# Kernel optimization log

Measured on AMD Instinct MI355X. Metric: run time of the kernel, lower is better.

## Reference

```python
import jax, jax.numpy as jnp
import numpy as np

B, S, D, H = 4, 2048, 1024, 16
HD = D // H  # head_dim = 64


def setup_inputs() -> dict:
    key = jax.random.key(0)
    ks = jax.random.split(key, 4)
    scale = 0.02
    return {
        "x": jax.random.normal(ks[0], (B, S, D), dtype=jnp.float32),
        "W_attn": jax.random.normal(ks[1], (D, 3 * D), dtype=jnp.float32) * scale,
        "b_attn": jnp.zeros((3 * D,), dtype=jnp.float32),
        "W_proj": jax.random.normal(ks[2], (D, D), dtype=jnp.float32) * scale,
        "b_proj": jnp.zeros((D,), dtype=jnp.float32),
    }


def reference(x, W_attn, b_attn, W_proj, b_proj):
    b, s, d = x.shape
    qkv = x @ W_attn + b_attn                      # [b, s, 3d]
    q, k, v = jnp.split(qkv, 3, axis=2)
    # [b, s, d] -> [b, h, s, hd]
    def to_heads(t):
        return t.reshape(b, s, H, HD).transpose(0, 2, 1, 3)
    q, k, v = to_heads(q), to_heads(k), to_heads(v)
    scores = jnp.einsum("bhqd,bhkd->bhqk", q, k) / jnp.sqrt(jnp.float32(HD))
    causal = jnp.tril(jnp.ones((s, s), dtype=bool))  # [s, s]
    scores = jnp.where(causal[None, None], scores, jnp.float32(-jnp.inf))
    probs = jax.nn.softmax(scores, axis=-1)
    y = jnp.einsum("bhqk,bhkd->bhqd", probs, v)    # [b, h, s, hd]
    y = y.transpose(0, 2, 1, 3).reshape(b, s, d)
    return y @ W_proj + b_proj
```

## Files before the change

### kernel.cpp

```cpp
#include <hip/hip_runtime.h>
#include <hip/hip_bf16.h>
#include <type_traits>

#define SQ    2048
#define DIM   1024
#define NH    16
#define HDIM  64
#define BATCH 4

typedef unsigned short u16;
typedef __bf16 bf16x8 __attribute__((ext_vector_type(8)));
typedef float  f32x4  __attribute__((ext_vector_type(4)));
typedef u16    u16x8  __attribute__((ext_vector_type(8)));

#define QSCALE 0.180336880f

__device__ __forceinline__ u16 f2bf(float f) {
  union { float f; unsigned u; } v; v.f = f;
  unsigned r = v.u + 0x7fffu + ((v.u >> 16) & 1u);
  return (u16)(r >> 16);
}

__device__ __forceinline__ float fast_exp2(float x) {
#if __has_builtin(__builtin_amdgcn_exp2f)
  return __builtin_amdgcn_exp2f(x);
#else
  float y;
  asm("v_exp_f32 %0, %1" : "=v"(y) : "v"(x));
  return y;
#endif
}

__device__ __forceinline__ void gll16(const u16* g, u16* l) {
  __builtin_amdgcn_global_load_lds((const __attribute__((address_space(1))) void*)g,
                                   (__attribute__((address_space(3))) void*)l,
                                   16, 0, 0);
}

__global__ __launch_bounds__(256)
void f32_to_bf16_vec(const float* __restrict__ in, u16* __restrict__ out, int n4)
{
  const int i = blockIdx.x * blockDim.x + threadIdx.x;
  if (i < n4) {
    const float4 v = ((const float4*)in)[i];
    ushort4 o;
    o.x = f2bf(v.x); o.y = f2bf(v.y); o.z = f2bf(v.z); o.w = f2bf(v.w);
    ((ushort4*)out)[i] = o;
  }
}

__global__ void transpose_f32_bf16(const float* __restrict__ in, u16* __restrict__ out,
                                   int R, int C)
{
  __shared__ u16 tile[32][33];
  const int bx = blockIdx.x * 32, by = blockIdx.y * 32;
  const int tx = threadIdx.x, ty = threadIdx.y;
  #pragma unroll
  for (int i = 0; i < 32; i += 8)
    tile[ty + i][tx] = f2bf(in[(size_t)(by + ty + i) * C + bx + tx]);
  __syncthreads();
  #pragma unroll
  for (int i = 0; i < 32; i += 8)
    out[(size_t)(bx + ty + i) * R + by + tx] = tile[tx][ty + i];
}

template<int MODE>
__global__ __launch_bounds__(256)
void gemm_bt(const u16* __restrict__ A, const u16* __restrict__ Bt,
             const float* __restrict__ bias, int K,
             u16* __restrict__ o0, u16* __restrict__ o1, float* __restrict__ of)
{
  __shared__ __align__(16) u16 A0[128 * 32], A1[128 * 32];
  __shared__ __align__(16) u16 B0[128 * 32], B1[128 * 32];

  const int t    = threadIdx.x;
  const int lane = t & 63, wave = t >> 6;
  const int l15  = lane & 15, quad = lane >> 4;
  const int wm   = (wave & 1) * 64, wn = (wave >> 1) * 64;
  const int m0   = blockIdx.y * 128, n0 = blockIdx.x * 128;

  const int srow = wave * 32 + (lane >> 2);
  const int scol = (lane & 3) * 8;

  f32x4 acc[4][4] = {};

  for (int k0 = 0; k0 < K; k0 += 64) {
    const u16* ga = A  + (size_t)(m0 + srow) * K + k0 + scol;
    const u16* gb = Bt + (size_t)(n0 + srow) * K + k0 + scol;
    gll16(ga,              &A0[(wave * 32)      * 32]);
    gll16(ga + 32,         &A1[(wave * 32)      * 32]);
    gll16(ga + 16 * K,     &A0[(wave * 32 + 16) * 32]);
    gll16(ga + 16 * K + 32,&A1[(wave * 32 + 16) * 32]);
    gll16(gb,              &B0[(wave * 32)      * 32]);
    gll16(gb + 32,         &B1[(wave * 32)      * 32]);
    gll16(gb + 16 * K,     &B0[(wave * 32 + 16) * 32]);
    gll16(gb + 16 * K + 32,&B1[(wave * 32 + 16) * 32]);
    __syncthreads();

    #pragma unroll
    for (int ks = 0; ks < 2; ++ks) {
      const u16* Als = ks ? A1 : A0;
      const u16* Bls = ks ? B1 : B0;
      bf16x8 af[4], bfr[4];
      #pragma unroll
      for (int i = 0; i < 4; ++i) af[i]  = *(const bf16x8*)&Als[(wm + 16*i + l15) * 32 + quad * 8];
      #pragma unroll
      for (int j = 0; j < 4; ++j) bfr[j] = *(const bf16x8*)&Bls[(wn + 16*j + l15) * 32 + quad * 8];
      #pragma unroll
      for (int i = 0; i < 4; ++i)
        #pragma unroll
        for (int j = 0; j < 4; ++j)
          acc[i][j] = (MODE == 2)
            ? __builtin_amdgcn_mfma_f32_16x16x32_bf16(bfr[j], af[i], acc[i][j], 0, 0, 0)
            : __builtin_amdgcn_mfma_f32_16x16x32_bf16(af[i], bfr[j], acc[i][j], 0, 0, 0);
    }
    __syncthreads();
  }

  if (MODE == 2) {
    #pragma unroll
    for (int j = 0; j < 4; ++j) {
      #pragma unroll
      for (int r = 0; r < 4; ++r) {
        const int d = n0 + wn + 16*j + quad * 4 + r;
        const float bn = bias[d];
        const int h = d >> 6, hd = d & 63;
        #pragma unroll
        for (int i = 0; i < 4; ++i) {
          const int m = m0 + wm + 16*i + l15;
          const int b = m >> 11, s = m & 2047;
          o0[(((size_t)(b * NH + h)) * HDIM + hd) * SQ + s] = f2bf(acc[i][j][r] + bn);
        }
      }
    }
  } else {
    #pragma unroll
    for (int j = 0; j < 4; ++j) {
      const int n = n0 + wn + 16*j + l15;
      const float bn = bias[n];
      #pragma unroll
      for (int i = 0; i < 4; ++i) {
        #pragma unroll
        for (int r = 0; r < 4; ++r) {
          const int m = m0 + wm + 16*i + quad * 4 + r;
          const float val = acc[i][j][r] + bn;
          if (MODE == 1) {
            const int sec = n >> 10, d = n & 1023;
            const int h = d >> 6, hd = d & 63;
            const int b = m >> 11, s = m & 2047;
            const int bh = b * NH + h;
            if (sec == 0) o0[((size_t)bh * SQ + s) * HDIM + hd] = f2bf(val * QSCALE);
            else          o1[((size_t)bh * SQ + s) * HDIM + hd] = f2bf(val);
          } else {
            of[(size_t)m * DIM + n] = val;
          }
        }
      }
    }
  }
}

__global__ __launch_bounds__(256)
void attn_fused(const u16* __restrict__ q_ws, const u16* __restrict__ k_ws,
                const u16* __restrict__ v_t, u16* __restrict__ y_ws)
{
  __shared__ __align__(16) u16 Kls[2][64 * 64];
  __shared__ __align__(16) u16 Vls[2][64 * 64];
  __shared__ __align__(16) u16 Pls[4][32 * 64];

  const int bh = blockIdx.x;
  const int p  = blockIdx.y;
  const int b = bh >> 4, h = bh & 15;
  const int t = threadIdx.x;
  const int lane = t & 63, wave = t >> 6;
  const int l15 = lane & 15, quad = lane >> 4;
  const int rx  = l15 & 7;
  const int cK0 = ((quad      ^ rx) << 3);
  const int cK1 = (((quad | 4) ^ rx) << 3);
  const int pswz = rx << 3;

  const u16* Q  = q_ws + (size_t)bh * SQ * HDIM;
  const u16* Kp = k_ws + (size_t)bh * SQ * HDIM;
  const u16* Vp = v_t  + (size_t)bh * HDIM * SQ;

  const int qtH = 15 - p, qtL = p;
  const int qrowH = qtH * 128 + wave * 32;
  const int qrowL = qtL * 128 + wave * 32;

  bf16x8 qf[4][2];
  #pragma unroll
  for (int qi = 0; qi < 2; ++qi)
    #pragma unroll
    for (int ks = 0; ks < 2; ++ks) {
      qf[qi][ks]     = *(const bf16x8*)&Q[(size_t)(qrowH + 16*qi + l15) * HDIM + ks * 32 + quad * 8];
      qf[2 + qi][ks] = *(const bf16x8*)&Q[(size_t)(qrowL + 16*qi + l15) * HDIM + ks * 32 + quad * 8];
    }

  f32x4 o[4][4] = {};
  float l_q[4] = {};

  const int r3   = lane >> 3;
  const int c8   = lane & 7;
  const int scol = ((c8 ^ r3) << 3);

  auto stage = [&](int kv0, int buf) {
    gll16(&Kp[(size_t)(kv0 + wave*16     + r3) * HDIM + scol], &Kls[buf][(wave*16    ) * 64]);
    gll16(&Kp[(size_t)(kv0 + wave*16 + 8 + r3) * HDIM + scol], &Kls[buf][(wave*16 + 8) * 64]);
    gll16(&Vp[(size_t)(wave*16     + r3) * SQ + kv0 + scol],   &Vls[buf][(wave*16    ) * 64]);
    gll16(&Vp[(size_t)(wave*16 + 8 + r3) * SQ + kv0 + scol],   &Vls[buf][(wave*16 + 8) * 64]);
  };

  auto compute = [&](int kv0, int buf, int base, int qrow, auto maskc) {
    constexpr bool MASKED = decltype(maskc)::value;
    f32x4 st[4][2] = {};
    const u16* Kb = Kls[buf];
    __builtin_amdgcn_s_setprio(1);
    #pragma unroll
    for (int ks = 0; ks < 2; ++ks) {
      const int cs = ks ? cK1 : cK0;
      #pragma unroll
      for (int kt = 0; kt < 4; ++kt) {
        bf16x8 kf = *(const bf16x8*)&Kb[(16*kt + l15) * 64 + cs];
        #pragma unroll
        for (int qi = 0; qi < 2; ++qi)
          st[kt][qi] = __builtin_amdgcn_mfma_f32_16x16x32_bf16(kf, qf[base + qi][ks], st[kt][qi], 0, 0, 0);
      }
    }
    __builtin_amdgcn_s_setprio(0);

    #pragma unroll
    for (int qi = 0; qi < 2; ++qi) {
      const int q = qrow + 16*qi + l15;
      float rsum = 0.f;
      #pragma unroll
      for (int kt = 0; kt < 4; ++kt)
        #pragma unroll
        for (int r = 0; r < 4; ++r) {
          float pv = fast_exp2(st[kt][qi][r]);
          if (MASKED && (kv0 + 16*kt + quad*4 + r) > q) pv = 0.f;
          st[kt][qi][r] = pv;
          rsum += pv;
        }
      l_q[base + qi] += rsum;
    }

    #pragma unroll
    for (int qi = 0; qi < 2; ++qi)
      #pragma unroll
      for (int kt = 0; kt < 4; ++kt) {
        union { __hip_bfloat162 h2[2]; ushort4 u4; } pk;
        pk.h2[0] = __float22bfloat162_rn(make_float2(st[kt][qi][0], st[kt][qi][1]));
        pk.h2[1] = __float22bfloat162_rn(make_float2(st[kt][qi][2], st[kt][qi][3]));
        *(ushort4*)&Pls[wave][(16*qi + l15) * 64 + ((16*kt + quad*4) ^ pswz)] = pk.u4;
      }

    const u16* Vb = Vls[buf];
    __builtin_amdgcn_s_setprio(1);
    #pragma unroll
    for (int ks = 0; ks < 2; ++ks) {
      const int cs = ks ? cK1 : cK0;
      bf16x8 vf[4];
      #pragma unroll
      for (int n = 0; n < 4; ++n)
        vf[n] = *(const bf16x8*)&Vb[(16*n + l15) * 64 + cs];
      #pragma unroll
      for (int mi = 0; mi < 2; ++mi) {
        bf16x8 pa = *(const bf16x8*)&Pls[wave][(16*mi + l15) * 64 + ((ks*32 + quad*8) ^ pswz)];
        #pragma unroll
        for (int n = 0; n < 4; ++n)
          o[base + mi][n] = __builtin_amdgcn_mfma_f32_16x16x32_bf16(pa, vf[n], o[base + mi][n], 0, 0, 0);
      }
    }
    __builtin_amdgcn_s_setprio(0);
  };

  const int ntiles = 2 * qtH + 2;
  const int lastH  = 2 * qtH + (wave >> 1);
  const int lastL  = 2 * qtL + (wave >> 1);

  stage(0, 0);
  for (int kvt = 0; kvt < ntiles; ++kvt) {
    const int cur = kvt & 1;
    const int kv0 = kvt * 64;
    __syncthreads();
    if (kvt + 1 < ntiles) stage((kvt + 1) * 64, cur ^ 1);
    if (kvt < lastH)       compute(kv0, cur, 0, qrowH, std::integral_constant<bool,false>{});
    else if (kvt == lastH) compute(kv0, cur, 0, qrowH, std::integral_constant<bool,true>{});
    if (kvt < lastL)       compute(kv0, cur, 2, qrowL, std::integral_constant<bool,false>{});
    else if (kvt == lastL) compute(kv0, cur, 2, qrowL, std::integral_constant<bool,true>{});
  }

  #pragma unroll
  for (int s = 0; s < 4; ++s) {
    l_q[s] += __shfl_xor(l_q[s], 16);
    l_q[s] += __shfl_xor(l_q[s], 32);
  }
  #pragma unroll
  for (int g = 0; g < 2; ++g) {
    const int qrow = g ? qrowL : qrowH;
    const int base = g * 2;
    #pragma unroll
    for (int mi = 0; mi < 2; ++mi)
      #pragma unroll
      for (int r = 0; r < 4; ++r) {
        const float lr = __shfl(l_q[base + mi], quad * 4 + r);
        const float inv = 1.0f / lr;
        const int qg = qrow + 16*mi + quad * 4 + r;
        #pragma unroll
        for (int n = 0; n < 4; ++n)
          y_ws[((size_t)b * SQ + qg) * DIM + h * HDIM + 16*n + l15] = f2bf(o[base + mi][n][r] * inv);
      }
  }
}

extern "C" void kernel_launch(void* const* d_in, const int* in_sizes, int n_in,
                              void* d_out, int out_size, void* d_ws, size_t ws_size,
                              hipStream_t stream)
{
  const float* x      = (const float*)d_in[0];
  const float* W_attn = (const float*)d_in[1];
  const float* b_attn = (const float*)d_in[2];
  const float* W_proj = (const float*)d_in[3];
  const float* b_proj = (const float*)d_in[4];
  float* out = (float*)d_out;

  char* ws = (char*)d_ws;
  u16* WattnT = (u16*)(ws);
  u16* WprojT = (u16*)(ws + 6291456);
  u16* xb     = (u16*)(ws + 8388608);
  u16* y_ws   = xb;
  u16* q_ws   = (u16*)(ws + 25165824);
  u16* k_ws   = (u16*)(ws + 41943040);
  u16* v_tw   = (u16*)(ws + 58720256);

  const dim3 tb(32, 8);
  transpose_f32_bf16<<<dim3(3 * DIM / 32, DIM / 32), tb, 0, stream>>>(W_attn, WattnT, DIM, 3 * DIM);
  transpose_f32_bf16<<<dim3(DIM / 32, DIM / 32), tb, 0, stream>>>(W_proj, WprojT, DIM, DIM);
  f32_to_bf16_vec<<<(BATCH * SQ * DIM / 4 + 255) / 256, 256, 0, stream>>>(x, xb, BATCH * SQ * DIM / 4);

  gemm_bt<1><<<dim3(2 * DIM / 128, BATCH * SQ / 128), 256, 0, stream>>>(
      xb, WattnT, b_attn, DIM, q_ws, k_ws, nullptr);
  gemm_bt<2><<<dim3(DIM / 128, BATCH * SQ / 128), 256, 0, stream>>>(
      xb, WattnT + (size_t)2048 * DIM, b_attn + 2048, DIM, v_tw, nullptr, nullptr);

  attn_fused<<<dim3(BATCH * NH, 8), 256, 0, stream>>>(q_ws, k_ws, v_tw, y_ws);

  gemm_bt<0><<<dim3(DIM / 128, BATCH * SQ / 128), 256, 0, stream>>>(
      y_ws, WprojT, b_proj, DIM, nullptr, nullptr, out);
}
```

Measured before the change: 259.2 us.

## Split attention block across eight waves with 16 query rows each

The attention kernel now launches 512 threads per block, and each of the eight waves handles 16 query rows per tile instead of 32. This halves per-wave register state and spreads the K/V staging across more waves. The compute call also processes the high and low query tiles in one fused call when both are active, sharing K and V fragment loads. The cost is a larger P scratch buffer in shared memory, more waves synchronising at the barrier, and fewer MFMAs per K fragment load within a wave.

New measurement: 258.5 us. About the same (-0.3%).

```diff
diff --git a/kernel.cpp b/kernel.cpp
--- a/kernel.cpp
+++ b/kernel.cpp
@@ -160,13 +160,13 @@
   }
 }
 
-__global__ __launch_bounds__(256)
+__global__ __launch_bounds__(512, 4)
 void attn_fused(const u16* __restrict__ q_ws, const u16* __restrict__ k_ws,
                 const u16* __restrict__ v_t, u16* __restrict__ y_ws)
 {
   __shared__ __align__(16) u16 Kls[2][64 * 64];
   __shared__ __align__(16) u16 Vls[2][64 * 64];
-  __shared__ __align__(16) u16 Pls[4][32 * 64];
+  __shared__ __align__(16) u16 Pls[8][32 * 64];
 
   const int bh = blockIdx.x;
   const int p  = blockIdx.y;
@@ -184,35 +184,33 @@
   const u16* Vp = v_t  + (size_t)bh * HDIM * SQ;
 
   const int qtH = 15 - p, qtL = p;
-  const int qrowH = qtH * 128 + wave * 32;
-  const int qrowL = qtL * 128 + wave * 32;
-
-  bf16x8 qf[4][2];
-  #pragma unroll
-  for (int qi = 0; qi < 2; ++qi)
-    #pragma unroll
-    for (int ks = 0; ks < 2; ++ks) {
-      qf[qi][ks]     = *(const bf16x8*)&Q[(size_t)(qrowH + 16*qi + l15) * HDIM + ks * 32 + quad * 8];
-      qf[2 + qi][ks] = *(const bf16x8*)&Q[(size_t)(qrowL + 16*qi + l15) * HDIM + ks * 32 + quad * 8];
-    }
-
-  f32x4 o[4][4] = {};
-  float l_q[4] = {};
+  const int qrowH = qtH * 128 + wave * 16;
+  const int qrowL = qtL * 128 + wave * 16;
+
+  bf16x8 qf[2][2];
+  #pragma unroll
+  for (int ks = 0; ks < 2; ++ks) {
+    qf[0][ks] = *(const bf16x8*)&Q[(size_t)(qrowH + l15) * HDIM + ks * 32 + quad * 8];
+    qf[1][ks] = *(const bf16x8*)&Q[(size_t)(qrowL + l15) * HDIM + ks * 32 + quad * 8];
+  }
+
+  f32x4 o[2][4] = {};
+  float l_q[2] = {};
 
   const int r3   = lane >> 3;
   const int c8   = lane & 7;
   const int scol = ((c8 ^ r3) << 3);
 
   auto stage = [&](int kv0, int buf) {
-    gll16(&Kp[(size_t)(kv0 + wave*16     + r3) * HDIM + scol], &Kls[buf][(wave*16    ) * 64]);
-    gll16(&Kp[(size_t)(kv0 + wave*16 + 8 + r3) * HDIM + scol], &Kls[buf][(wave*16 + 8) * 64]);
-    gll16(&Vp[(size_t)(wave*16     + r3) * SQ + kv0 + scol],   &Vls[buf][(wave*16    ) * 64]);
-    gll16(&Vp[(size_t)(wave*16 + 8 + r3) * SQ + kv0 + scol],   &Vls[buf][(wave*16 + 8) * 64]);
+    gll16(&Kp[(size_t)(kv0 + wave*8 + r3) * HDIM + scol], &Kls[buf][(wave*8) * 64]);
+    gll16(&Vp[(size_t)(wave*8 + r3) * SQ + kv0 + scol],   &Vls[buf][(wave*8) * 64]);
   };
 
-  auto compute = [&](int kv0, int buf, int base, int qrow, auto maskc) {
-    constexpr bool MASKED = decltype(maskc)::value;
-    f32x4 st[4][2] = {};
+  auto compute = [&](int kv0, int buf, auto doLc, auto mHc, auto mLc) {
+    constexpr bool DO_L = decltype(doLc)::value;
+    constexpr bool MH   = decltype(mHc)::value;
+    constexpr bool ML   = decltype(mLc)::value;
+    f32x4 st[2][4] = {};
     const u16* Kb = Kls[buf];
     __builtin_amdgcn_s_setprio(1);
     #pragma unroll
@@ -221,38 +219,58 @@
       #pragma unroll
       for (int kt = 0; kt < 4; ++kt) {
         bf16x8 kf = *(const bf16x8*)&Kb[(16*kt + l15) * 64 + cs];
-        #pragma unroll
-        for (int qi = 0; qi < 2; ++qi)
-          st[kt][qi] = __builtin_amdgcn_mfma_f32_16x16x32_bf16(kf, qf[base + qi][ks], st[kt][qi], 0, 0, 0);
+        st[0][kt] = __builtin_amdgcn_mfma_f32_16x16x32_bf16(kf, qf[0][ks], st[0][kt], 0, 0, 0);
+        if (DO_L)
+          st[1][kt] = __builtin_amdgcn_mfma_f32_16x16x32_bf16(kf, qf[1][ks], st[1][kt], 0, 0, 0);
       }
     }
     __builtin_amdgcn_s_setprio(0);
 
-    #pragma unroll
-    for (int qi = 0; qi < 2; ++qi) {
-      const int q = qrow + 16*qi + l15;
+    {
+      const int q = qrowH + l15;
       float rsum = 0.f;
       #pragma unroll
       for (int kt = 0; kt < 4; ++kt)
         #pragma unroll
         for (int r = 0; r < 4; ++r) {
-          float pv = fast_exp2(st[kt][qi][r]);
-          if (MASKED && (kv0 + 16*kt + quad*4 + r) > q) pv = 0.f;
-          st[kt][qi][r] = pv;
+          float pv = fast_exp2(st[0][kt][r]);
+          if (MH && (kv0 + 16*kt + quad*4 + r) > q) pv = 0.f;
+          st[0][kt][r] = pv;
           rsum += pv;
         }
-      l_q[base + qi] += rsum;
-    }
-
-    #pragma unroll
-    for (int qi = 0; qi < 2; ++qi)
+      l_q[0] += rsum;
+    }
+    if (DO_L) {
+      const int q = qrowL + l15;
+      float rsum = 0.f;
+      #pragma unroll
+      for (int kt = 0; kt < 4; ++kt)
+        #pragma unroll
+        for (int r = 0; r < 4; ++r) {
+          float pv = fast_exp2(st[1][kt][r]);
+          if (ML && (kv0 + 16*kt + quad*4 + r) > q) pv = 0.f;
+          st[1][kt][r] = pv;
+          rsum += pv;
+        }
+      l_q[1] += rsum;
+    }
+
+    #pragma unroll
+    for (int kt = 0; kt < 4; ++kt) {
+      union { __hip_bfloat162 h2[2]; ushort4 u4; } pk;
+      pk.h2[0] = __float22bfloat162_rn(make_float2(st[0][kt][0], st[0][kt][1]));
+      pk.h2[1] = __float22bfloat162_rn(make_float2(st[0][kt][2], st[0][kt][3]));
+      *(ushort4*)&Pls[wave][l15 * 64 + ((16*kt + quad*4) ^ pswz)] = pk.u4;
+    }
+    if (DO_L) {
       #pragma unroll
       for (int kt = 0; kt < 4; ++kt) {
         union { __hip_bfloat162 h2[2]; ushort4 u4; } pk;
-        pk.h2[0] = __float22bfloat162_rn(make_float2(st[kt][qi][0], st[kt][qi][1]));
-        pk.h2[1] = __float22bfloat162_rn(make_float2(st[kt][qi][2], st[kt][qi][3]));
-        *(ushort4*)&Pls[wave][(16*qi + l15) * 64 + ((16*kt + quad*4) ^ pswz)] = pk.u4;
-      }
+        pk.h2[0] = __float22bfloat162_rn(make_float2(st[1][kt][0], st[1][kt][1]));
+        pk.h2[1] = __float22bfloat162_rn(make_float2(st[1][kt][2], st[1][kt][3]));
+        *(ushort4*)&Pls[wave][(16 + l15) * 64 + ((16*kt + quad*4) ^ pswz)] = pk.u4;
+      }
+    }
 
     const u16* Vb = Vls[buf];
     __builtin_amdgcn_s_setprio(1);
@@ -263,20 +281,26 @@
       #pragma unroll
       for (int n = 0; n < 4; ++n)
         vf[n] = *(const bf16x8*)&Vb[(16*n + l15) * 64 + cs];
-      #pragma unroll
-      for (int mi = 0; mi < 2; ++mi) {
-        bf16x8 pa = *(const bf16x8*)&Pls[wave][(16*mi + l15) * 64 + ((ks*32 + quad*8) ^ pswz)];
+      bf16x8 pa0 = *(const bf16x8*)&Pls[wave][l15 * 64 + ((ks*32 + quad*8) ^ pswz)];
+      #pragma unroll
+      for (int n = 0; n < 4; ++n)
+        o[0][n] = __builtin_amdgcn_mfma_f32_16x16x32_bf16(pa0, vf[n], o[0][n], 0, 0, 0);
+      if (DO_L) {
+        bf16x8 pa1 = *(const bf16x8*)&Pls[wave][(16 + l15) * 64 + ((ks*32 + quad*8) ^ pswz)];
         #pragma unroll
         for (int n = 0; n < 4; ++n)
-          o[base + mi][n] = __builtin_amdgcn_mfma_f32_16x16x32_bf16(pa, vf[n], o[base + mi][n], 0, 0, 0);
+          o[1][n] = __builtin_amdgcn_mfma_f32_16x16x32_bf16(pa1, vf[n], o[1][n], 0, 0, 0);
       }
     }
     __builtin_amdgcn_s_setprio(0);
   };
 
   const int ntiles = 2 * qtH + 2;
-  const int lastH  = 2 * qtH + (wave >> 1);
-  const int lastL  = 2 * qtL + (wave >> 1);
+  const int lastH  = 2 * qtH + (wave >> 2);
+  const int lastL  = 2 * qtL + (wave >> 2);
+
+  using Fc = std::integral_constant<bool, false>;
+  using Tc = std::integral_constant<bool, true>;
 
   stage(0, 0);
   for (int kvt = 0; kvt < ntiles; ++kvt) {
@@ -284,32 +308,29 @@
     const int kv0 = kvt * 64;
     __syncthreads();
     if (kvt + 1 < ntiles) stage((kvt + 1) * 64, cur ^ 1);
-    if (kvt < lastH)       compute(kv0, cur, 0, qrowH, std::integral_constant<bool,false>{});
-    else if (kvt == lastH) compute(kv0, cur, 0, qrowH, std::integral_constant<bool,true>{});
-    if (kvt < lastL)       compute(kv0, cur, 2, qrowL, std::integral_constant<bool,false>{});
-    else if (kvt == lastL) compute(kv0, cur, 2, qrowL, std::integral_constant<bool,true>{});
-  }
-
-  #pragma unroll
-  for (int s = 0; s < 4; ++s) {
+    if      (kvt <  lastL) compute(kv0, cur, Tc{}, Fc{}, Fc{});
+    else if (kvt == lastL) compute(kv0, cur, Tc{}, Fc{}, Tc{});
+    else if (kvt <  lastH) compute(kv0, cur, Fc{}, Fc{}, Fc{});
+    else if (kvt == lastH) compute(kv0, cur, Fc{}, Tc{}, Fc{});
+  }
+
+  #pragma unroll
+  for (int s = 0; s < 2; ++s) {
     l_q[s] += __shfl_xor(l_q[s], 16);
     l_q[s] += __shfl_xor(l_q[s], 32);
   }
   #pragma unroll
   for (int g = 0; g < 2; ++g) {
     const int qrow = g ? qrowL : qrowH;
-    const int base = g * 2;
-    #pragma unroll
-    for (int mi = 0; mi < 2; ++mi)
-      #pragma unroll
-      for (int r = 0; r < 4; ++r) {
-        const float lr = __shfl(l_q[base + mi], quad * 4 + r);
-        const float inv = 1.0f / lr;
-        const int qg = qrow + 16*mi + quad * 4 + r;
-        #pragma unroll
-        for (int n = 0; n < 4; ++n)
-          y_ws[((size_t)b * SQ + qg) * DIM + h * HDIM + 16*n + l15] = f2bf(o[base + mi][n][r] * inv);
-      }
+    #pragma unroll
+    for (int r = 0; r < 4; ++r) {
+      const float lr = __shfl(l_q[g], quad * 4 + r);
+      const float inv = 1.0f / lr;
+      const int qg = qrow + quad * 4 + r;
+      #pragma unroll
+      for (int n = 0; n < 4; ++n)
+        y_ws[((size_t)b * SQ + qg) * DIM + h * HDIM + 16*n + l15] = f2bf(o[g][n][r] * inv);
+    }
   }
 }
 
@@ -343,7 +364,7 @@
   gemm_bt<2><<<dim3(DIM / 128, BATCH * SQ / 128), 256, 0, stream>>>(
       xb, WattnT + (size_t)2048 * DIM, b_attn + 2048, DIM, v_tw, nullptr, nullptr);
 
-  attn_fused<<<dim3(BATCH * NH, 8), 256, 0, stream>>>(q_ws, k_ws, v_tw, y_ws);
+  attn_fused<<<dim3(BATCH * NH, 8), 512, 0, stream>>>(q_ws, k_ws, v_tw, y_ws);
 
   gemm_bt<0><<<dim3(DIM / 128, BATCH * SQ / 128), 256, 0, stream>>>(
       y_ws, WprojT, b_proj, DIM, nullptr, nullptr, out);
```
